# Kernel tuning notes

Measured on AMD Instinct MI355X. Metric: run time of the kernel, lower is better.

Reference implementation:

```python
import jax, jax.numpy as jnp
import numpy as np

N_NODES = 100000
N_EDGES = 3200000
F_IN = 256
HEADS = 8
C_OUT = 8
NEG_SLOPE = 0.2


def setup_inputs() -> dict:
    key = jax.random.key(0)
    k1, k2, k3, k4, k5, k6 = jax.random.split(key, 6)
    x = jax.random.normal(k1, (N_NODES, F_IN), dtype=jnp.float32)
    edge_index = jax.random.randint(k2, (2, N_EDGES), 0, N_NODES, dtype=jnp.int64)
    W = jax.random.normal(k3, (F_IN, HEADS * C_OUT), dtype=jnp.float32) * (1.0 / np.sqrt(F_IN))
    att_src = jax.random.normal(k4, (HEADS, C_OUT), dtype=jnp.float32) * 0.1
    att_dst = jax.random.normal(k5, (HEADS, C_OUT), dtype=jnp.float32) * 0.1
    bias = jax.random.normal(k6, (HEADS * C_OUT,), dtype=jnp.float32) * 0.01
    return {"x": x, "edge_index": edge_index, "W": W, "att_src": att_src, "att_dst": att_dst, "bias": bias}


def reference(x, edge_index, W, att_src, att_dst, bias):
    # GATConv (PyG semantics), concat=True, inference (dropout off).
    N = x.shape[0]
    H, C = att_src.shape
    h = (x @ W).reshape(N, H, C)                      # [N,H,C] transformed features
    a_src = jnp.einsum('nhc,hc->nh', h, att_src)      # [N,H]
    a_dst = jnp.einsum('nhc,hc->nh', h, att_dst)      # [N,H]
    src, dst = edge_index[0], edge_index[1]
    # per-edge raw attention logits
    e = jax.nn.leaky_relu(a_src[src] + a_dst[dst], NEG_SLOPE)  # [E,H]
    # segment softmax over incoming edges of each destination node
    m = jax.ops.segment_max(e, dst, num_segments=N)            # [N,H]
    e = jnp.exp(e - m[dst])
    s = jax.ops.segment_sum(e, dst, num_segments=N)            # [N,H]
    alpha = e / (s[dst] + 1e-16)                               # [E,H]
    # scatter-add weighted neighbor features
    out = jax.ops.segment_sum(alpha[:, :, None] * h[src], dst, num_segments=N)  # [N,H,C]
    return out.reshape(N, H * C) + bias
```

## Files before the change

### kernel.cpp

```cpp
#include <hip/hip_runtime.h>
#include <hip/hip_fp16.h>
#include <math.h>

#define F_IN 256
#define HC 64
#define NHEAD 8
#define NEG 0.2f
#define BSH 7
#define BSZ 128
#define CAP 5376

__global__ __launch_bounds__(256) void k_gemm(
    const float* __restrict__ x, const float* __restrict__ W,
    const float* __restrict__ att_src, const float* __restrict__ att_dst,
    __half2* __restrict__ h2, float* __restrict__ asrc, float* __restrict__ adst, int N) {
  __shared__ float Wl[128 * HC];
  int t = threadIdx.x;
  int g = t >> 4, q = t & 15;
  int c0 = q * 4, hd = q >> 1, cb = c0 & 7;
  float as0 = att_src[hd * 8 + cb + 0], as1 = att_src[hd * 8 + cb + 1];
  float as2 = att_src[hd * 8 + cb + 2], as3 = att_src[hd * 8 + cb + 3];
  float ad0 = att_dst[hd * 8 + cb + 0], ad1 = att_dst[hd * 8 + cb + 1];
  float ad2 = att_dst[hd * 8 + cb + 2], ad3 = att_dst[hd * 8 + cb + 3];

  int nb = blockIdx.x * 128 + g * 8;
  const float* xr[8];
#pragma unroll
  for (int i = 0; i < 8; i++) {
    int id = nb + i;
    if (id > N - 1) id = N - 1;
    xr[i] = x + (size_t)id * F_IN;
  }
  float4 acc[8];
#pragma unroll
  for (int i = 0; i < 8; i++) acc[i] = make_float4(0.f, 0.f, 0.f, 0.f);

  for (int half = 0; half < 2; half++) {
    __syncthreads();
    for (int i = t * 4; i < 128 * HC; i += 1024)
      *(float4*)&Wl[i] = *(const float4*)&W[half * 128 * HC + i];
    __syncthreads();
    int kb = half * 128;
    for (int k = 0; k < 128; k += 4) {
      float4 w0 = *(float4*)&Wl[(k + 0) * HC + c0];
      float4 w1 = *(float4*)&Wl[(k + 1) * HC + c0];
      float4 w2 = *(float4*)&Wl[(k + 2) * HC + c0];
      float4 w3 = *(float4*)&Wl[(k + 3) * HC + c0];
#pragma unroll
      for (int i = 0; i < 8; i++) {
        float4 xv = *(const float4*)(xr[i] + kb + k);
        acc[i].x = fmaf(xv.x, w0.x, fmaf(xv.y, w1.x, fmaf(xv.z, w2.x, fmaf(xv.w, w3.x, acc[i].x))));
        acc[i].y = fmaf(xv.x, w0.y, fmaf(xv.y, w1.y, fmaf(xv.z, w2.y, fmaf(xv.w, w3.y, acc[i].y))));
        acc[i].z = fmaf(xv.x, w0.z, fmaf(xv.y, w1.z, fmaf(xv.z, w2.z, fmaf(xv.w, w3.z, acc[i].z))));
        acc[i].w = fmaf(xv.x, w0.w, fmaf(xv.y, w1.w, fmaf(xv.z, w2.w, fmaf(xv.w, w3.w, acc[i].w))));
      }
    }
  }

#pragma unroll
  for (int i = 0; i < 8; i++) {
    float ps = acc[i].x * as0 + acc[i].y * as1 + acc[i].z * as2 + acc[i].w * as3;
    float pd = acc[i].x * ad0 + acc[i].y * ad1 + acc[i].z * ad2 + acc[i].w * ad3;
    ps += __shfl_xor(ps, 1);
    pd += __shfl_xor(pd, 1);
    int id = nb + i;
    if (id < N) {
      union { uint2 u; __half2 p[2]; } pk;
      pk.p[0] = __halves2half2(__float2half_rn(acc[i].x), __float2half_rn(acc[i].y));
      pk.p[1] = __halves2half2(__float2half_rn(acc[i].z), __float2half_rn(acc[i].w));
      *(uint2*)(h2 + (size_t)id * 32 + (c0 >> 1)) = pk.u;
      if (!(q & 1)) {
        asrc[id * NHEAD + hd] = ps;
        adst[id * NHEAD + hd] = pd;
      }
    }
  }
}

__global__ void k_zero(int* __restrict__ p, int n) {
  int i = blockIdx.x * 256 + threadIdx.x;
  if (i < n) p[i] = 0;
}

__global__ __launch_bounds__(512) void k_partition(
    const int* __restrict__ edge, int* __restrict__ bcursor,
    unsigned int* __restrict__ entries, int E, int NB) {
  __shared__ unsigned long long srt8[8192];
  __shared__ int hist[1024];
  __shared__ int loff[1024];
  __shared__ int basearr[1024];
  __shared__ int pr[512];
  int t = threadIdx.x;
  int base = blockIdx.x * 8192;
  int cblk = min(8192, E - base);
  for (int i = t; i < 1024; i += 512) hist[i] = 0;
  __syncthreads();
#pragma unroll
  for (int j = 0; j < 16; j++) {
    int e = base + j * 512 + t;
    if (e < E) atomicAdd(&hist[edge[E + e] >> BSH], 1);
  }
  __syncthreads();
  int a = hist[2 * t], b = hist[2 * t + 1];
  pr[t] = a + b;
  __syncthreads();
  for (int off = 1; off < 512; off <<= 1) {
    int add = (t >= off) ? pr[t - off] : 0;
    __syncthreads();
    pr[t] += add;
    __syncthreads();
  }
  int excl = pr[t] - (a + b);
  loff[2 * t] = excl;
  loff[2 * t + 1] = excl + a;
  if (a > 0 && 2 * t < NB) basearr[2 * t] = atomicAdd(&bcursor[2 * t], a);
  if (b > 0 && 2 * t + 1 < NB) basearr[2 * t + 1] = atomicAdd(&bcursor[2 * t + 1], b);
  hist[2 * t] = excl;
  hist[2 * t + 1] = excl + a;
  __syncthreads();
#pragma unroll
  for (int j = 0; j < 16; j++) {
    int e = base + j * 512 + t;
    if (e < E) {
      int s = edge[e], d = edge[E + e];
      int p = atomicAdd(&hist[d >> BSH], 1);
      srt8[p] = ((unsigned long long)(unsigned int)d << 32) | (unsigned int)s;
    }
  }
  __syncthreads();
  for (int i = t; i < cblk; i += 512) {
    unsigned long long v = srt8[i];
    int d = (int)(v >> 32), s = (int)(v & 0xFFFFFFFFu);
    int bk = d >> BSH;
    int local = basearr[bk] + (i - loff[bk]);
    if (local < CAP)
      entries[(size_t)bk * CAP + local] = ((unsigned int)(d & (BSZ - 1)) << 17) | (unsigned int)s;
  }
}

__global__ __launch_bounds__(512, 6) void k_bagg(
    const unsigned int* __restrict__ entries, const int* __restrict__ bcursor,
    const __half2* __restrict__ h2, const float* __restrict__ asrc,
    const float* __restrict__ adst, const float* __restrict__ bias,
    float* __restrict__ out, int N) {
  __shared__ int srt[CAP];
  __shared__ int hist[BSZ];
  __shared__ int cur[BSZ];
  __shared__ int off[BSZ + 1];
  __shared__ int tmp[BSZ];
  int t = threadIdx.x;
  int bkt = blockIdx.x;
  int n0 = bkt << BSH;
  int ncnt = min(BSZ, N - n0);
  int cnt = bcursor[bkt];
  if (cnt > CAP) cnt = CAP;
  const unsigned int* ebase = entries + (size_t)bkt * CAP;
  for (int i = t; i < BSZ; i += 512) hist[i] = 0;
  __syncthreads();
  for (int i = t; i < cnt; i += 512)
    atomicAdd(&hist[ebase[i] >> 17], 1);
  __syncthreads();
  if (t < BSZ) tmp[t] = hist[t];
  __syncthreads();
  for (int o = 1; o < BSZ; o <<= 1) {
    int add = (t < BSZ && t >= o) ? tmp[t - o] : 0;
    __syncthreads();
    if (t < BSZ) tmp[t] += add;
    __syncthreads();
  }
  if (t < BSZ) { off[t] = tmp[t] - hist[t]; cur[t] = tmp[t] - hist[t]; }
  if (t == 0) off[BSZ] = cnt;
  __syncthreads();
  for (int i = t; i < cnt; i += 512) {
    unsigned int v = ebase[i];
    int p = atomicAdd(&cur[v >> 17], 1);
    srt[p] = (int)(v & 0x1FFFF);
  }
  __syncthreads();
  int wv = t >> 6, lane = t & 63;
  int sub = lane >> 5, sl = lane & 31;
  int head = sl >> 2;
  for (int nd = wv; nd < ncnt; nd += 8) {
    int node = n0 + nd;
    int sbeg = off[nd], send = off[nd + 1];
    float ad = adst[node * NHEAD + head];
    float ax = 0.f, ay = 0.f, wsum = 0.f;
    int k = sbeg + sub;
    for (; k + 6 < send; k += 8) {
      int s0 = srt[k];
      int s1 = srt[k + 2];
      int s2 = srt[k + 4];
      int s3 = srt[k + 6];
      float l0 = asrc[s0 * NHEAD + head] + ad;
      float l1 = asrc[s1 * NHEAD + head] + ad;
      float l2 = asrc[s2 * NHEAD + head] + ad;
      float l3 = asrc[s3 * NHEAD + head] + ad;
      __half2 v0 = h2[(size_t)s0 * 32 + sl];
      __half2 v1 = h2[(size_t)s1 * 32 + sl];
      __half2 v2 = h2[(size_t)s2 * 32 + sl];
      __half2 v3 = h2[(size_t)s3 * 32 + sl];
      float w0 = __expf(fmaxf(l0, NEG * l0));
      float w1 = __expf(fmaxf(l1, NEG * l1));
      float w2 = __expf(fmaxf(l2, NEG * l2));
      float w3 = __expf(fmaxf(l3, NEG * l3));
      float2 f0 = __half22float2(v0);
      float2 f1 = __half22float2(v1);
      float2 f2 = __half22float2(v2);
      float2 f3 = __half22float2(v3);
      ax = fmaf(w0, f0.x, fmaf(w1, f1.x, fmaf(w2, f2.x, fmaf(w3, f3.x, ax))));
      ay = fmaf(w0, f0.y, fmaf(w1, f1.y, fmaf(w2, f2.y, fmaf(w3, f3.y, ay))));
      wsum += (w0 + w1) + (w2 + w3);
    }
    for (; k < send; k += 2) {
      int s = srt[k];
      float lg = asrc[s * NHEAD + head] + ad;
      float w = __expf(fmaxf(lg, NEG * lg));
      float2 f = __half22float2(h2[(size_t)s * 32 + sl]);
      ax = fmaf(w, f.x, ax);
      ay = fmaf(w, f.y, ay);
      wsum += w;
    }
    ax += __shfl_xor(ax, 32);
    ay += __shfl_xor(ay, 32);
    wsum += __shfl_xor(wsum, 32);
    if (sub == 0) {
      float inv = wsum > 0.f ? 1.0f / wsum : 0.f;
      float2 bx = *(const float2*)&bias[2 * sl];
      float2 r;
      r.x = fmaf(ax, inv, bx.x);
      r.y = fmaf(ay, inv, bx.y);
      *(float2*)&out[(size_t)node * HC + 2 * sl] = r;
    }
  }
}

extern "C" void kernel_launch(void* const* d_in, const int* in_sizes, int n_in,
                              void* d_out, int out_size, void* d_ws, size_t ws_size,
                              hipStream_t stream) {
  const float* x = (const float*)d_in[0];
  const int* edge = (const int*)d_in[1];
  const float* W = (const float*)d_in[2];
  const float* att_src = (const float*)d_in[3];
  const float* att_dst = (const float*)d_in[4];
  const float* bias = (const float*)d_in[5];
  int N = in_sizes[0] / F_IN;
  int E = in_sizes[1] / 2;
  float* out = (float*)d_out;
  int NB = (N + BSZ - 1) >> BSH;

  __half2* h2 = (__half2*)d_ws;
  float* asrc = (float*)(h2 + (size_t)N * 32);
  float* adst = asrc + (size_t)N * NHEAD;
  int* bcursor = (int*)(adst + (size_t)N * NHEAD);
  unsigned int* entries = (unsigned int*)(bcursor + NB);

  int nch = (E + 8191) / 8192;

  k_zero<<<(NB + 255) / 256, 256, 0, stream>>>(bcursor, NB);
  k_gemm<<<(N + 127) / 128, 256, 0, stream>>>(x, W, att_src, att_dst, h2, asrc, adst, N);
  k_partition<<<nch, 512, 0, stream>>>(edge, bcursor, entries, E, NB);
  k_bagg<<<NB, 512, 0, stream>>>(entries, bcursor, h2, asrc, adst, bias, out, N);
}
```

Measured before the change: 370.4 us.

## Compute node projection GEMM with split-bf16 MFMA instead of FP32 FMA

Replaces the scalar FP32 FMA GEMM (x @ W) with MFMA bf16 16x16x32 instructions. Each operand is split into high and low bf16 parts and three products are summed to keep near-FP32 accuracy. A new prep kernel pre-splits and swizzles W into an MFMA-friendly layout and also zeroes the bucket cursors, replacing the separate zero kernel. The attention dot products are computed from the MFMA output layout with cross-lane shuffles. The risks are extra shuffle and conversion work, plus small precision differences from dropping the lo*lo term.

```diff
diff --git a/kernel.cpp b/kernel.cpp
--- a/kernel.cpp
+++ b/kernel.cpp
@@ -10,76 +10,135 @@
 #define BSZ 128
 #define CAP 5376
 
-__global__ __launch_bounds__(256) void k_gemm(
-    const float* __restrict__ x, const float* __restrict__ W,
+typedef __attribute__((ext_vector_type(8))) short bf16x8;
+typedef __attribute__((ext_vector_type(4))) float f32x4;
+
+union BV { uint4 q; bf16x8 v; };
+
+__device__ __forceinline__ unsigned int hi_pair(float a, float b) {
+  return (__float_as_uint(b) & 0xffff0000u) | (__float_as_uint(a) >> 16);
+}
+__device__ __forceinline__ unsigned int lo_pair(float a, float b) {
+  float ra = a - __uint_as_float(__float_as_uint(a) & 0xffff0000u);
+  float rb = b - __uint_as_float(__float_as_uint(b) & 0xffff0000u);
+  return (__float_as_uint(rb) & 0xffff0000u) | (__float_as_uint(ra) >> 16);
+}
+
+__global__ __launch_bounds__(256) void k_prep(const float* __restrict__ W,
+                                              unsigned short* __restrict__ Wp,
+                                              int* __restrict__ bcursor, int NB) {
+  int b = blockIdx.x, t = threadIdx.x;
+  if (b >= 64) {
+    int i = (b - 64) * 256 + t;
+    if (i < NB) bcursor[i] = 0;
+    return;
+  }
+  int idx = b * 256 + t;
+  int k = idx >> 6, c = idx & 63;
+  float w = W[idx];
+  unsigned int u = __float_as_uint(w);
+  unsigned short hi = (unsigned short)((u + 0x7fffu + ((u >> 16) & 1u)) >> 16);
+  float r = w - __uint_as_float((unsigned int)hi << 16);
+  unsigned int ur = __float_as_uint(r);
+  unsigned short lo = (unsigned short)((ur + 0x7fffu + ((ur >> 16) & 1u)) >> 16);
+  int ks = k >> 5, j = k & 7, lg = (k >> 3) & 3;
+  int lane = lg * 16 + (c & 15), cg = c >> 4;
+  int off = ((ks * 4 + cg) * 64 + lane) * 8 + j;
+  Wp[off] = hi;
+  Wp[16384 + off] = lo;
+}
+
+__global__ __launch_bounds__(256, 3) void k_gemm(
+    const float* __restrict__ x, const uint4* __restrict__ Wp4,
     const float* __restrict__ att_src, const float* __restrict__ att_dst,
     __half2* __restrict__ h2, float* __restrict__ asrc, float* __restrict__ adst, int N) {
-  __shared__ float Wl[128 * HC];
   int t = threadIdx.x;
-  int g = t >> 4, q = t & 15;
-  int c0 = q * 4, hd = q >> 1, cb = c0 & 7;
-  float as0 = att_src[hd * 8 + cb + 0], as1 = att_src[hd * 8 + cb + 1];
-  float as2 = att_src[hd * 8 + cb + 2], as3 = att_src[hd * 8 + cb + 3];
-  float ad0 = att_dst[hd * 8 + cb + 0], ad1 = att_dst[hd * 8 + cb + 1];
-  float ad2 = att_dst[hd * 8 + cb + 2], ad3 = att_dst[hd * 8 + cb + 3];
-
-  int nb = blockIdx.x * 128 + g * 8;
-  const float* xr[8];
-#pragma unroll
-  for (int i = 0; i < 8; i++) {
-    int id = nb + i;
-    if (id > N - 1) id = N - 1;
-    xr[i] = x + (size_t)id * F_IN;
-  }
-  float4 acc[8];
-#pragma unroll
-  for (int i = 0; i < 8; i++) acc[i] = make_float4(0.f, 0.f, 0.f, 0.f);
-
-  for (int half = 0; half < 2; half++) {
-    __syncthreads();
-    for (int i = t * 4; i < 128 * HC; i += 1024)
-      *(float4*)&Wl[i] = *(const float4*)&W[half * 128 * HC + i];
-    __syncthreads();
-    int kb = half * 128;
-    for (int k = 0; k < 128; k += 4) {
-      float4 w0 = *(float4*)&Wl[(k + 0) * HC + c0];
-      float4 w1 = *(float4*)&Wl[(k + 1) * HC + c0];
-      float4 w2 = *(float4*)&Wl[(k + 2) * HC + c0];
-      float4 w3 = *(float4*)&Wl[(k + 3) * HC + c0];
-#pragma unroll
-      for (int i = 0; i < 8; i++) {
-        float4 xv = *(const float4*)(xr[i] + kb + k);
-        acc[i].x = fmaf(xv.x, w0.x, fmaf(xv.y, w1.x, fmaf(xv.z, w2.x, fmaf(xv.w, w3.x, acc[i].x))));
-        acc[i].y = fmaf(xv.x, w0.y, fmaf(xv.y, w1.y, fmaf(xv.z, w2.y, fmaf(xv.w, w3.y, acc[i].y))));
-        acc[i].z = fmaf(xv.x, w0.z, fmaf(xv.y, w1.z, fmaf(xv.z, w2.z, fmaf(xv.w, w3.z, acc[i].z))));
-        acc[i].w = fmaf(xv.x, w0.w, fmaf(xv.y, w1.w, fmaf(xv.z, w2.w, fmaf(xv.w, w3.w, acc[i].w))));
+  int wv = t >> 6, l = t & 63;
+  int lr = l & 15, lg = l >> 4;
+  int r0 = blockIdx.x * 128 + wv * 32;
+  int ra = r0 + lr;      if (ra > N - 1) ra = N - 1;
+  int rb = r0 + 16 + lr; if (rb > N - 1) rb = N - 1;
+  const float* xr0 = x + (size_t)ra * F_IN + lg * 8;
+  const float* xr1 = x + (size_t)rb * F_IN + lg * 8;
+  const uint4* wp = Wp4 + l;
+
+  float as4[4], ad4[4];
+#pragma unroll
+  for (int cg = 0; cg < 4; cg++) {
+    as4[cg] = att_src[cg * 16 + lr];
+    ad4[cg] = att_dst[cg * 16 + lr];
+  }
+
+  f32x4 acc[2][4];
+#pragma unroll
+  for (int i = 0; i < 2; i++)
+#pragma unroll
+    for (int j = 0; j < 4; j++) acc[i][j] = (f32x4){0.f, 0.f, 0.f, 0.f};
+
+#pragma unroll
+  for (int ks = 0; ks < 8; ks++) {
+    float4 p0 = *(const float4*)(xr0 + ks * 32);
+    float4 q0 = *(const float4*)(xr0 + ks * 32 + 4);
+    float4 p1 = *(const float4*)(xr1 + ks * 32);
+    float4 q1 = *(const float4*)(xr1 + ks * 32 + 4);
+    BV bh[4], bl[4];
+#pragma unroll
+    for (int cg = 0; cg < 4; cg++) {
+      bh[cg].q = wp[(ks * 4 + cg) * 64];
+      bl[cg].q = wp[2048 + (ks * 4 + cg) * 64];
+    }
+    BV ah0, al0, ah1, al1;
+    ah0.q.x = hi_pair(p0.x, p0.y); ah0.q.y = hi_pair(p0.z, p0.w);
+    ah0.q.z = hi_pair(q0.x, q0.y); ah0.q.w = hi_pair(q0.z, q0.w);
+    al0.q.x = lo_pair(p0.x, p0.y); al0.q.y = lo_pair(p0.z, p0.w);
+    al0.q.z = lo_pair(q0.x, q0.y); al0.q.w = lo_pair(q0.z, q0.w);
+    ah1.q.x = hi_pair(p1.x, p1.y); ah1.q.y = hi_pair(p1.z, p1.w);
+    ah1.q.z = hi_pair(q1.x, q1.y); ah1.q.w = hi_pair(q1.z, q1.w);
+    al1.q.x = lo_pair(p1.x, p1.y); al1.q.y = lo_pair(p1.z, p1.w);
+    al1.q.z = lo_pair(q1.x, q1.y); al1.q.w = lo_pair(q1.z, q1.w);
+#pragma unroll
+    for (int cg = 0; cg < 4; cg++) {
+      acc[0][cg] = __builtin_amdgcn_mfma_f32_16x16x32_bf16(ah0.v, bh[cg].v, acc[0][cg], 0, 0, 0);
+      acc[0][cg] = __builtin_amdgcn_mfma_f32_16x16x32_bf16(al0.v, bh[cg].v, acc[0][cg], 0, 0, 0);
+      acc[0][cg] = __builtin_amdgcn_mfma_f32_16x16x32_bf16(ah0.v, bl[cg].v, acc[0][cg], 0, 0, 0);
+      acc[1][cg] = __builtin_amdgcn_mfma_f32_16x16x32_bf16(ah1.v, bh[cg].v, acc[1][cg], 0, 0, 0);
+      acc[1][cg] = __builtin_amdgcn_mfma_f32_16x16x32_bf16(al1.v, bh[cg].v, acc[1][cg], 0, 0, 0);
+      acc[1][cg] = __builtin_amdgcn_mfma_f32_16x16x32_bf16(ah1.v, bl[cg].v, acc[1][cg], 0, 0, 0);
+    }
+  }
+
+#pragma unroll
+  for (int rg = 0; rg < 2; rg++) {
+#pragma unroll
+    for (int tt = 0; tt < 4; tt++) {
+      int node = r0 + rg * 16 + 4 * lg + tt;
+      bool ok = node < N;
+      float v0 = acc[rg][0][tt], v1 = acc[rg][1][tt], v2 = acc[rg][2][tt], v3 = acc[rg][3][tt];
+      float o0 = __shfl_xor(v0, 1), o1 = __shfl_xor(v1, 1);
+      float o2 = __shfl_xor(v2, 1), o3 = __shfl_xor(v3, 1);
+      if (ok && !(l & 1)) {
+        size_t hb = (size_t)node * 32 + (lr >> 1);
+        h2[hb]      = __halves2half2(__float2half_rn(v0), __float2half_rn(o0));
+        h2[hb + 8]  = __halves2half2(__float2half_rn(v1), __float2half_rn(o1));
+        h2[hb + 16] = __halves2half2(__float2half_rn(v2), __float2half_rn(o2));
+        h2[hb + 24] = __halves2half2(__float2half_rn(v3), __float2half_rn(o3));
       }
-    }
-  }
-
-#pragma unroll
-  for (int i = 0; i < 8; i++) {
-    float ps = acc[i].x * as0 + acc[i].y * as1 + acc[i].z * as2 + acc[i].w * as3;
-    float pd = acc[i].x * ad0 + acc[i].y * ad1 + acc[i].z * ad2 + acc[i].w * ad3;
-    ps += __shfl_xor(ps, 1);
-    pd += __shfl_xor(pd, 1);
-    int id = nb + i;
-    if (id < N) {
-      union { uint2 u; __half2 p[2]; } pk;
-      pk.p[0] = __halves2half2(__float2half_rn(acc[i].x), __float2half_rn(acc[i].y));
-      pk.p[1] = __halves2half2(__float2half_rn(acc[i].z), __float2half_rn(acc[i].w));
-      *(uint2*)(h2 + (size_t)id * 32 + (c0 >> 1)) = pk.u;
-      if (!(q & 1)) {
-        asrc[id * NHEAD + hd] = ps;
-        adst[id * NHEAD + hd] = pd;
+#pragma unroll
+      for (int cg = 0; cg < 4; cg++) {
+        float v = (cg == 0) ? v0 : (cg == 1) ? v1 : (cg == 2) ? v2 : v3;
+        float s = v * as4[cg];
+        float d = v * ad4[cg];
+        s += __shfl_xor(s, 1); d += __shfl_xor(d, 1);
+        s += __shfl_xor(s, 2); d += __shfl_xor(d, 2);
+        s += __shfl_xor(s, 4); d += __shfl_xor(d, 4);
+        if (ok && !(l & 7)) {
+          int hd = 2 * cg + (lr >> 3);
+          asrc[node * NHEAD + hd] = s;
+          adst[node * NHEAD + hd] = d;
+        }
       }
     }
   }
-}
-
-__global__ void k_zero(int* __restrict__ p, int n) {
-  int i = blockIdx.x * 256 + threadIdx.x;
-  if (i < n) p[i] = 0;
 }
 
 __global__ __launch_bounds__(512) void k_partition(
@@ -248,16 +307,18 @@
   float* out = (float*)d_out;
   int NB = (N + BSZ - 1) >> BSH;
 
-  __half2* h2 = (__half2*)d_ws;
+  unsigned short* Wp = (unsigned short*)d_ws;
+  __half2* h2 = (__half2*)((char*)d_ws + 65536);
   float* asrc = (float*)(h2 + (size_t)N * 32);
   float* adst = asrc + (size_t)N * NHEAD;
   int* bcursor = (int*)(adst + (size_t)N * NHEAD);
-  unsigned int* entries = (unsigned int*)(bcursor + NB);
+  unsigned int* entries = (unsigned int*)(bcursor + ((NB + 3) & ~3));
 
   int nch = (E + 8191) / 8192;
-
-  k_zero<<<(NB + 255) / 256, 256, 0, stream>>>(bcursor, NB);
-  k_gemm<<<(N + 127) / 128, 256, 0, stream>>>(x, W, att_src, att_dst, h2, asrc, adst, N);
+  int nzb = (NB + 255) / 256;
+
+  k_prep<<<64 + nzb, 256, 0, stream>>>(W, Wp, bcursor, NB);
+  k_gemm<<<(N + 127) / 128, 256, 0, stream>>>(x, (const uint4*)Wp, att_src, att_dst, h2, asrc, adst, N);
   k_partition<<<nch, 512, 0, stream>>>(edge, bcursor, entries, E, NB);
   k_bagg<<<NB, 512, 0, stream>>>(entries, bcursor, h2, asrc, adst, bias, out, N);
 }
```

New measurement: 330.4 us. -10.8%, faster.
